# Optimization experiments

Hardware: AMD Instinct MI355X
Metric: run time of the kernel (lower is better)

The kernel has to match this reference:

```python
import jax, jax.numpy as jnp
import numpy as np

B, N, DIM = 4, 1024, 768
HEADS, DIM_HEAD = 12, 64
INNER = HEADS * DIM_HEAD  # 768
SCALE = DIM ** -0.5


def setup_inputs() -> dict:
    key = jax.random.key(0)
    ks = jax.random.split(key, 5)
    return {
        "x": jax.random.normal(ks[0], (B, N, DIM), dtype=jnp.float32),
        "pos_embedding": jax.random.normal(ks[1], (B, N, DIM), dtype=jnp.float32),
        "w_qkv": jax.random.normal(ks[2], (DIM, 3 * INNER), dtype=jnp.float32) * (DIM ** -0.5),
        "w_qk_pos": jax.random.normal(ks[3], (DIM, 2 * INNER), dtype=jnp.float32) * (DIM ** -0.5),
        "w_out": jax.random.normal(ks[4], (INNER, DIM), dtype=jnp.float32) * (INNER ** -0.5),
        "b_out": jnp.zeros((DIM,), dtype=jnp.float32),
    }


def _split_heads(t):
    # [b, n, h*d] -> [b, h, n, d]
    b, n, _ = t.shape
    return t.reshape(b, n, HEADS, DIM_HEAD).transpose(0, 2, 1, 3)


def reference(x, pos_embedding, w_qkv, w_qk_pos, w_out, b_out):
    qkv = x @ w_qkv  # [b, n, 3*inner]
    q, k, v = (_split_heads(t) for t in jnp.split(qkv, 3, axis=-1))
    qk_pos = pos_embedding @ w_qk_pos  # [b, n, 2*inner]
    q_pos, k_pos = (_split_heads(t) for t in jnp.split(qk_pos, 2, axis=-1))

    dots = jnp.einsum('bhid,bhjd->bhij', q, k) * SCALE
    dots_pos = jnp.einsum('bhid,bhjd->bhij', q_pos, k_pos) * SCALE
    dots = (dots + dots_pos) * 0.5  # averaged content+positional scores

    attn = jax.nn.softmax(dots, axis=-1)
    out = jnp.einsum('bhij,bhjd->bhid', attn, v)
    out = out.transpose(0, 2, 1, 3).reshape(x.shape[0], x.shape[1], INNER)
    return out @ w_out + b_out
```

## Files before the change

### kernel.cpp

```cpp
#include <hip/hip_runtime.h>
#include <cstdint>
#include <cstddef>

typedef __bf16 bf16;
typedef __bf16 bf16x8 __attribute__((ext_vector_type(8)));
typedef __bf16 bf16x4v __attribute__((ext_vector_type(4)));
typedef float  f32x4  __attribute__((ext_vector_type(4)));

#define MFMA(a, b, c) __builtin_amdgcn_mfma_f32_16x16x32_bf16((a), (b), (c), 0, 0, 0)

typedef __attribute__((address_space(3))) unsigned int  lds_u32;
typedef __attribute__((address_space(1))) unsigned int glob_u32;


__global__ void k_prep(const float* __restrict__ x, const float* __restrict__ pos,
                       const float* __restrict__ w_qkv, const float* __restrict__ w_qk_pos,
                       const float* __restrict__ w_out,
                       bf16* __restrict__ xb, bf16* __restrict__ posb,
                       bf16* __restrict__ wqkvT, bf16* __restrict__ wqkposT,
                       bf16* __restrict__ woutT) {
    __shared__ float t[32][33];
    const int blk = blockIdx.x;
    if (blk < 6144) {
        int i = blk * 256 + threadIdx.x;
        const float* in = x; bf16* out = xb;
        if (i >= 786432) { i -= 786432; in = pos; out = posb; }
        float4 v = reinterpret_cast<const float4*>(in)[i];
        bf16x4v o; o[0] = (bf16)v.x; o[1] = (bf16)v.y; o[2] = (bf16)v.z; o[3] = (bf16)v.w;
        reinterpret_cast<bf16x4v*>(out)[i] = o;
        return;
    }
    int bx = (blk - 6144) % 144, ky = (blk - 6144) / 144;
    const float* in; bf16* out; int N;
    if (bx < 72)       { in = w_qkv;    out = wqkvT;   N = 2304; }
    else if (bx < 120) { in = w_qk_pos; out = wqkposT; N = 1536; bx -= 72; }
    else               { in = w_out;    out = woutT;   N = 768;  bx -= 120; }
    const int n0 = bx * 32, k0 = ky * 32;
    const int tx = threadIdx.x & 31, ty = threadIdx.x >> 5;
#pragma unroll
    for (int r = 0; r < 32; r += 8)
        t[ty + r][tx] = in[(size_t)(k0 + ty + r) * N + n0 + tx];
    __syncthreads();
#pragma unroll
    for (int r = 0; r < 32; r += 8)
        out[(size_t)(n0 + ty + r) * 768 + k0 + tx] = (bf16)t[tx][ty + r];
}

__launch_bounds__(512, 2)
__global__ void k_gemm12(const bf16* __restrict__ xb, const bf16* __restrict__ posb,
                         const bf16* __restrict__ wqkvT, const bf16* __restrict__ wqkposT,
                         bf16* __restrict__ qcat, bf16* __restrict__ kcat,
                         bf16* __restrict__ vT) {
    __shared__ bf16 lA[2][256][32];
    __shared__ bf16 lB[2][256][32];

    const int tid  = threadIdx.x;
    const int lane = tid & 63, wave = tid >> 6;
    const int quad = lane >> 4, col = lane & 15;
    const int sw2  = (col >> 1) & 3;
    const int wm = (wave >> 2) * 128, wn = (wave & 3) * 64;

    const int fid = blockIdx.x;
    const int xcd = fid & 7, s = fid >> 3;
    const int bx = s % 15;
    const int by = xcd * 2 + s / 15;

    int mode, nBase;
    const bf16 *A, *BT;
    if (bx < 9) { mode = 0; A = xb;   BT = wqkvT;   nBase = bx * 256; }
    else        { mode = 1; A = posb; BT = wqkposT; nBase = (bx - 9) * 256; }
    const int mBase = by * 256;

    const bf16* Ap = A  + (size_t)mBase * 768;
    const bf16* Bp = BT + (size_t)nBase * 768;

#define STAGE12(buf, k0)                                                        \
    _Pragma("unroll")                                                           \
    for (int j = 0; j < 2; ++j) {                                               \
        int idx = (wave * 2 + j) * 64 + lane;                                   \
        int row = idx >> 2, c = (idx & 3) ^ ((row >> 1) & 3);                   \
        __builtin_amdgcn_global_load_lds(                                       \
            (const glob_u32*)(Ap + (size_t)row * 768 + (k0) + c * 8),           \
            (lds_u32*)((char*)&lA[buf][0][0] + (wave * 2 + j) * 1024), 16, 0, 0);\
        __builtin_amdgcn_global_load_lds(                                       \
            (const glob_u32*)(Bp + (size_t)row * 768 + (k0) + c * 8),           \
            (lds_u32*)((char*)&lB[buf][0][0] + (wave * 2 + j) * 1024), 16, 0, 0);\
    }

    f32x4 acc[8][4];
#pragma unroll
    for (int mi = 0; mi < 8; ++mi)
#pragma unroll
        for (int ni = 0; ni < 4; ++ni) acc[mi][ni] = f32x4{0.f, 0.f, 0.f, 0.f};

    STAGE12(0, 0)
    for (int it = 0; it < 24; ++it) {
        const int cur = it & 1, nxt = cur ^ 1;
        __syncthreads();
        if (it < 23) STAGE12(nxt, (it + 1) * 32)

        bf16x8 af[8], bfg[4];
#pragma unroll
        for (int mi = 0; mi < 8; ++mi)
            af[mi]  = *(const bf16x8*)&lA[cur][wm + mi * 16 + col][(quad ^ sw2) * 8];
#pragma unroll
        for (int ni = 0; ni < 4; ++ni)
            bfg[ni] = *(const bf16x8*)&lB[cur][wn + ni * 16 + col][(quad ^ sw2) * 8];
#pragma unroll
        for (int mi = 0; mi < 8; ++mi)
#pragma unroll
            for (int ni = 0; ni < 4; ++ni)
                acc[mi][ni] = MFMA(af[mi], bfg[ni], acc[mi][ni]);
    }
#undef STAGE12

    const float c2s = 0.018042195912f * 1.44269504089f;
    const int bb = mBase >> 10;
    const int sr0 = (mBase & 1023) + wm + quad * 4;
    const int which = (mode == 0) ? (nBase >= 1536 ? 2 : (nBase >= 768 ? 1 : 0))
                                  : (nBase >= 768 ? 1 : 0);
#pragma unroll
    for (int ni = 0; ni < 4; ++ni) {
        const int nb = nBase + wn + ni * 16;
        const int rem = nb - which * 768;
        const int hh = rem >> 6, dd0 = rem & 63;
        const size_t hb = (size_t)(bb * 12 + hh);
        if (mode == 0 && which == 2) {
            bf16* dstv = vT + (hb * 64 + dd0 + col) * 1024 + sr0;
#pragma unroll
            for (int mi = 0; mi < 8; ++mi) {
                bf16x4v pk;
#pragma unroll
                for (int r = 0; r < 4; ++r) pk[r] = (bf16)acc[mi][ni][r];
                *(bf16x4v*)(dstv + mi * 16) = pk;
            }
        } else {
            const float scl = (which == 0) ? c2s : 1.0f;
            bf16* dstq = (which == 0 ? qcat : kcat)
                       + (hb * 1024 + sr0) * 128 + (mode == 1 ? 64 : 0) + dd0 + col;
#pragma unroll
            for (int mi = 0; mi < 8; ++mi)
#pragma unroll
                for (int r = 0; r < 4; ++r)
                    dstq[(size_t)(mi * 16 + r) * 128] = (bf16)(acc[mi][ni][r] * scl);
        }
    }
}

__launch_bounds__(256, 3)
__global__ void k_attn(const bf16* __restrict__ qcat, const bf16* __restrict__ kcat,
                       const bf16* __restrict__ vT, bf16* __restrict__ attn_out) {
    __shared__ bf16 lK[2][64][128];
    __shared__ bf16 lV[2][64][72];

    const int tid  = threadIdx.x;
    const int lane = tid & 63, wave = tid >> 6;
    const int quad = lane >> 4, col = lane & 15;
    const int sw   = col & 7;

    const int fid = blockIdx.x;
    const int xcd = fid & 7, s = fid >> 3;
    const int qt = s & 15;
    const int unit = (s >> 4) * 8 + xcd;
    const int b = unit / 12, h = unit % 12;

    const bf16* Qb = qcat + (size_t)unit * 1024 * 128;
    const bf16* Kb = kcat + (size_t)unit * 1024 * 128;
    const bf16* Vb = vT   + (size_t)unit * 64 * 1024;

    const int kidx = wave * 256 + lane;

#define STAGE_K(buf, kv0)                                                      \
    _Pragma("unroll")                                                          \
    for (int j = 0; j < 4; ++j) {                                              \
        int idx = kidx + j * 64;                                               \
        int row = idx >> 4, c = idx & 15, csrc = c ^ (row & 7);                \
        __builtin_amdgcn_global_load_lds(                                      \
            (const glob_u32*)(Kb + (size_t)((kv0) + row) * 128 + csrc * 8),    \
            (lds_u32*)(&lK[buf][0][0] + (wave * 4 + j) * 512), 16, 0, 0);      \
    }

    int vdj[2], vsk[2], vka[2];
#pragma unroll
    for (int j = 0; j < 2; ++j) {
        int cid = wave * 128 + j * 64 + lane;
        vdj[j] = cid >> 3;
        int sck = cid & 7;
        vsk[j] = sck * 8;
        vka[j] = (sck >> 2) * 32 + (sck & 1) * 16 + ((sck >> 1) & 1) * 4;
    }

#define LOAD_V(kv0)                                                            \
    _Pragma("unroll")                                                          \
    for (int j = 0; j < 2; ++j)                                                \
        vreg[j] = *(const uint4*)(Vb + (size_t)vdj[j] * 1024 + (kv0) + vsk[j]);
#define WRITE_V(buf)                                                           \
    _Pragma("unroll")                                                          \
    for (int j = 0; j < 2; ++j) {                                               \
        *(uint2*)&lV[buf][vdj[j]][vka[j]]     = make_uint2(vreg[j].x, vreg[j].y);\
        *(uint2*)&lV[buf][vdj[j]][vka[j] + 8] = make_uint2(vreg[j].z, vreg[j].w);\
    }

    bf16x8 qb[4];
    {
        const bf16* qrow = Qb + (size_t)(qt * 64 + wave * 16 + col) * 128;
#pragma unroll
        for (int f = 0; f < 4; ++f) qb[f] = *(const bf16x8*)(qrow + f * 32 + quad * 8);
    }

    f32x4 o[4];
#pragma unroll
    for (int vt = 0; vt < 4; ++vt) o[vt] = f32x4{0.f, 0.f, 0.f, 0.f};
    float lsum = 0.f;

    uint4 vreg[2];
    STAGE_K(0, 0)
    LOAD_V(0)
    WRITE_V(0)

    for (int it = 0; it < 16; ++it) {
        const int cur = it & 1, nxt = cur ^ 1;
        __syncthreads();
        if (it < 15) {
            const int kv1 = (it + 1) * 64;
            STAGE_K(nxt, kv1)
            LOAD_V(kv1)
        }

        f32x4 st[4];
#pragma unroll
        for (int t = 0; t < 4; ++t) st[t] = f32x4{0.f, 0.f, 0.f, 0.f};
#pragma unroll
        for (int t = 0; t < 4; ++t)
#pragma unroll
            for (int f = 0; f < 4; ++f) {
                bf16x8 kf = *(const bf16x8*)&lK[cur][t * 16 + col][((f * 4 + quad) ^ sw) * 8];
                st[t] = MFMA(kf, qb[f], st[t]);
            }

        bf16x8 pbf[2];
#pragma unroll
        for (int c = 0; c < 2; ++c) {
#pragma unroll
            for (int r = 0; r < 4; ++r) {
                float p0 = exp2f(st[2 * c][r]);
                float p1 = exp2f(st[2 * c + 1][r]);
                lsum += p0 + p1;
                pbf[c][r]     = (bf16)p0;
                pbf[c][4 + r] = (bf16)p1;
            }
        }

#pragma unroll
        for (int c = 0; c < 2; ++c)
#pragma unroll
            for (int vt = 0; vt < 4; ++vt) {
                bf16x8 vf = *(const bf16x8*)&lV[cur][vt * 16 + col][c * 32 + quad * 8];
                o[vt] = MFMA(vf, pbf[c], o[vt]);
            }

        if (it < 15) WRITE_V(nxt)
    }

    float l = lsum;
    l += __shfl_xor(l, 16, 64);
    l += __shfl_xor(l, 32, 64);
    const float inv = 1.f / l;

    const int qrow = qt * 64 + wave * 16 + col;
    bf16* dst = attn_out + ((size_t)b * 1024 + qrow) * 768 + h * 64;
#pragma unroll
    for (int vt = 0; vt < 4; ++vt) {
        bf16x4v pk;
#pragma unroll
        for (int r = 0; r < 4; ++r) pk[r] = (bf16)(o[vt][r] * inv);
        *(bf16x4v*)(dst + vt * 16 + quad * 4) = pk;
    }
#undef STAGE_K
#undef LOAD_V
#undef WRITE_V
}

__launch_bounds__(256, 3)
__global__ void k_gemm_out(const bf16* __restrict__ aout, const bf16* __restrict__ woutT,
                           const float* __restrict__ bias, float* __restrict__ out) {
    __shared__ bf16 lA[2][64][32];
    __shared__ bf16 lB[2][64][32];

    const int tid  = threadIdx.x;
    const int lane = tid & 63, wave = tid >> 6;
    const int quad = lane >> 4, col = lane & 15;
    const int sw2  = (col >> 1) & 3;
    const int wm = (wave >> 1) * 32, wn = (wave & 1) * 32;

    const int fid = blockIdx.x;
    const int xcd = fid & 7, s = fid >> 3;
    const int bx = s % 12;
    const int by = xcd * 8 + s / 12;

    const int mBase = by * 64, nBase = bx * 64;

    const bf16* Ap = aout  + (size_t)mBase * 768;
    const bf16* Bp = woutT + (size_t)nBase * 768;

#define STAGE_O(buf, k0)                                                        \
    {                                                                           \
        int idx = wave * 64 + lane;                                             \
        int row = idx >> 2, c = (idx & 3) ^ ((row >> 1) & 3);                   \
        __builtin_amdgcn_global_load_lds(                                       \
            (const glob_u32*)(Ap + (size_t)row * 768 + (k0) + c * 8),           \
            (lds_u32*)((char*)&lA[buf][0][0] + wave * 1024), 16, 0, 0);         \
        __builtin_amdgcn_global_load_lds(                                       \
            (const glob_u32*)(Bp + (size_t)row * 768 + (k0) + c * 8),           \
            (lds_u32*)((char*)&lB[buf][0][0] + wave * 1024), 16, 0, 0);         \
    }

    f32x4 acc[2][2];
#pragma unroll
    for (int mi = 0; mi < 2; ++mi)
#pragma unroll
        for (int ni = 0; ni < 2; ++ni) acc[mi][ni] = f32x4{0.f, 0.f, 0.f, 0.f};

    STAGE_O(0, 0)
    for (int it = 0; it < 24; ++it) {
        const int cur = it & 1, nxt = cur ^ 1;
        __syncthreads();
        if (it < 23) STAGE_O(nxt, (it + 1) * 32)

        bf16x8 af[2], bfg[2];
#pragma unroll
        for (int mi = 0; mi < 2; ++mi)
            af[mi]  = *(const bf16x8*)&lA[cur][wm + mi * 16 + col][(quad ^ sw2) * 8];
#pragma unroll
        for (int ni = 0; ni < 2; ++ni)
            bfg[ni] = *(const bf16x8*)&lB[cur][wn + ni * 16 + col][(quad ^ sw2) * 8];
#pragma unroll
        for (int mi = 0; mi < 2; ++mi)
#pragma unroll
            for (int ni = 0; ni < 2; ++ni)
                acc[mi][ni] = MFMA(af[mi], bfg[ni], acc[mi][ni]);
    }
#undef STAGE_O

#pragma unroll
    for (int mi = 0; mi < 2; ++mi)
#pragma unroll
        for (int ni = 0; ni < 2; ++ni)
#pragma unroll
            for (int r = 0; r < 4; ++r) {
                int m = mBase + wm + mi * 16 + quad * 4 + r;
                int n = nBase + wn + ni * 16 + col;
                out[(size_t)m * 768 + n] = acc[mi][ni][r] + bias[n];
            }
}

extern "C" void kernel_launch(void* const* d_in, const int* in_sizes, int n_in,
                              void* d_out, int out_size, void* d_ws, size_t ws_size,
                              hipStream_t stream) {
    const float* x        = (const float*)d_in[0];
    const float* pos      = (const float*)d_in[1];
    const float* w_qkv    = (const float*)d_in[2];
    const float* w_qk_pos = (const float*)d_in[3];
    const float* w_out    = (const float*)d_in[4];
    const float* b_out    = (const float*)d_in[5];
    float* out = (float*)d_out;

    char* ws = (char*)d_ws;
    bf16* xb      = (bf16*)(ws);
    bf16* posb    = (bf16*)(ws + 6291456);
    bf16* wqkvT   = (bf16*)(ws + 12582912);
    bf16* wqkposT = (bf16*)(ws + 16121856);
    bf16* woutT   = (bf16*)(ws + 18481152);
    bf16* qcat    = (bf16*)(ws + 19660800);
    bf16* kcat    = (bf16*)(ws + 32243712);
    bf16* vT      = (bf16*)(ws + 44826624);
    bf16* aout    = (bf16*)(ws + 51118080);

    k_prep<<<9600, 256, 0, stream>>>(x, pos, w_qkv, w_qk_pos, w_out,
                                     xb, posb, wqkvT, wqkposT, woutT);
    k_gemm12<<<240, 512, 0, stream>>>(xb, posb, wqkvT, wqkposT, qcat, kcat, vT);
    k_attn<<<768, 256, 0, stream>>>(qcat, kcat, vT, aout);
    k_gemm_out<<<768, 256, 0, stream>>>(aout, woutT, b_out, out);
}
```

Before: 182.3 us.

## Restructure QKV projection GEMM into 8-wave ping-pong pipeline with quadrant-split LDS

Rewrites the main loop of the QKV/positional projection GEMM. The K step grows from 32 to 64 and the LDS tiles are split into halves, so each wave loads its A/B quadrant fragments and issues MFMA sub-blocks between explicit barriers, while global-to-LDS loads for later K tiles are spread across the phases. This is meant to overlap global loads, LDS reads and MFMA more finely than the old double-buffer loop. Separately, s_setprio is raised around MFMA clusters in both the GEMM and the attention kernel to favour matrix issue. The barrier and waitcnt choreography is complex and a mistake could cause data races, and the many barriers add sync overhead.

```diff
diff --git a/kernel.cpp b/kernel.cpp
--- a/kernel.cpp
+++ b/kernel.cpp
@@ -51,14 +51,18 @@
                          const bf16* __restrict__ wqkvT, const bf16* __restrict__ wqkposT,
                          bf16* __restrict__ qcat, bf16* __restrict__ kcat,
                          bf16* __restrict__ vT) {
-    __shared__ bf16 lA[2][256][32];
-    __shared__ bf16 lB[2][256][32];
+    __shared__ bf16 lA[2][2][2][128][32];
+    __shared__ bf16 lB[2][2][2][128][32];
 
     const int tid  = threadIdx.x;
     const int lane = tid & 63, wave = tid >> 6;
     const int quad = lane >> 4, col = lane & 15;
     const int sw2  = (col >> 1) & 3;
-    const int wm = (wave >> 2) * 128, wn = (wave & 3) * 64;
+    const int rg8  = (quad ^ sw2) * 8;
+    const int mh   = wave >> 2;
+    const int nh   = (wave >> 1) & 1;
+    const int nb64 = (wave & 1) * 64;
+    const int wm   = mh * 128, wn = (wave & 3) * 64;
 
     const int fid = blockIdx.x;
     const int xcd = fid & 7, s = fid >> 3;
@@ -74,18 +78,53 @@
     const bf16* Ap = A  + (size_t)mBase * 768;
     const bf16* Bp = BT + (size_t)nBase * 768;
 
-#define STAGE12(buf, k0)                                                        \
-    _Pragma("unroll")                                                           \
-    for (int j = 0; j < 2; ++j) {                                               \
-        int idx = (wave * 2 + j) * 64 + lane;                                   \
-        int row = idx >> 2, c = (idx & 3) ^ ((row >> 1) & 3);                   \
-        __builtin_amdgcn_global_load_lds(                                       \
-            (const glob_u32*)(Ap + (size_t)row * 768 + (k0) + c * 8),           \
-            (lds_u32*)((char*)&lA[buf][0][0] + (wave * 2 + j) * 1024), 16, 0, 0);\
-        __builtin_amdgcn_global_load_lds(                                       \
-            (const glob_u32*)(Bp + (size_t)row * 768 + (k0) + c * 8),           \
-            (lds_u32*)((char*)&lB[buf][0][0] + (wave * 2 + j) * 1024), 16, 0, 0);\
-    }
+#define STAGE_A8(ss, h, t)                                                     \
+    _Pragma("unroll")                                                          \
+    for (int j = 0; j < 2; ++j) {                                              \
+        int c = (lane & 3) ^ ((lane >> 3) & 3);                                \
+        __builtin_amdgcn_global_load_lds(                                      \
+            (const glob_u32*)(Ap + (size_t)((h) * 128 + wave * 16 + (lane >> 2)) * 768 \
+                              + (t) * 64 + j * 32 + c * 8),                    \
+            (lds_u32*)(&lA[ss][h][j][wave * 16][0]), 16, 0, 0);                \
+    }
+#define STAGE_B8(ss, h, t)                                                     \
+    _Pragma("unroll")                                                          \
+    for (int j = 0; j < 2; ++j) {                                              \
+        int c = (lane & 3) ^ ((lane >> 3) & 3);                                \
+        __builtin_amdgcn_global_load_lds(                                      \
+            (const glob_u32*)(Bp + (size_t)((h) * 128 + wave * 16 + (lane >> 2)) * 768 \
+                              + (t) * 64 + j * 32 + c * 8),                    \
+            (lds_u32*)(&lB[ss][h][j][wave * 16][0]), 16, 0, 0);                \
+    }
+
+#define READ_A8(ss, mq)                                                        \
+    _Pragma("unroll")                                                          \
+    for (int f = 0; f < 4; ++f)                                                \
+    _Pragma("unroll")                                                          \
+    for (int ks = 0; ks < 2; ++ks)                                             \
+        afr[f][ks] = *(const bf16x8*)&lA[ss][mh][ks][(mq) * 64 + f * 16 + col][rg8];
+#define READ_B8(ss, nq)                                                        \
+    _Pragma("unroll")                                                          \
+    for (int n = 0; n < 2; ++n)                                                \
+    _Pragma("unroll")                                                          \
+    for (int ks = 0; ks < 2; ++ks)                                             \
+        bfr[n][ks] = *(const bf16x8*)&lB[ss][nh][ks][nb64 + (nq) * 32 + n * 16 + col][rg8];
+
+#define MM16(mq, nq)                                                           \
+    __builtin_amdgcn_s_setprio(1);                                             \
+    _Pragma("unroll")                                                          \
+    for (int ks = 0; ks < 2; ++ks)                                             \
+    _Pragma("unroll")                                                          \
+    for (int f = 0; f < 4; ++f)                                                \
+    _Pragma("unroll")                                                          \
+    for (int n = 0; n < 2; ++n)                                                \
+        acc[(mq) * 4 + f][(nq) * 2 + n] =                                      \
+            MFMA(afr[f][ks], bfr[n][ks], acc[(mq) * 4 + f][(nq) * 2 + n]);     \
+    __builtin_amdgcn_s_setprio(0);
+
+#define BAR()   __builtin_amdgcn_s_barrier()
+#define LGKM0() do { asm volatile("s_waitcnt lgkmcnt(0)" ::: "memory");        \
+                     __builtin_amdgcn_sched_barrier(0); } while (0)
 
     f32x4 acc[8][4];
 #pragma unroll
@@ -93,26 +132,65 @@
 #pragma unroll
         for (int ni = 0; ni < 4; ++ni) acc[mi][ni] = f32x4{0.f, 0.f, 0.f, 0.f};
 
-    STAGE12(0, 0)
-    for (int it = 0; it < 24; ++it) {
-        const int cur = it & 1, nxt = cur ^ 1;
-        __syncthreads();
-        if (it < 23) STAGE12(nxt, (it + 1) * 32)
-
-        bf16x8 af[8], bfg[4];
-#pragma unroll
-        for (int mi = 0; mi < 8; ++mi)
-            af[mi]  = *(const bf16x8*)&lA[cur][wm + mi * 16 + col][(quad ^ sw2) * 8];
-#pragma unroll
-        for (int ni = 0; ni < 4; ++ni)
-            bfg[ni] = *(const bf16x8*)&lB[cur][wn + ni * 16 + col][(quad ^ sw2) * 8];
-#pragma unroll
-        for (int mi = 0; mi < 8; ++mi)
-#pragma unroll
-            for (int ni = 0; ni < 4; ++ni)
-                acc[mi][ni] = MFMA(af[mi], bfg[ni], acc[mi][ni]);
-    }
-#undef STAGE12
+    bf16x8 afr[4][2], bfr[2][2];
+
+    STAGE_A8(0, 0, 0) STAGE_A8(0, 1, 0)
+    STAGE_B8(0, 0, 0)
+    STAGE_B8(0, 1, 0)
+    STAGE_A8(1, 0, 1) STAGE_A8(1, 1, 1)
+    asm volatile("s_waitcnt vmcnt(4)" ::: "memory");
+    BAR();
+
+    for (int i = 0; i < 6; ++i) {
+        const int tO = 2 * i + 1, tE2 = 2 * i + 2, tO2 = 2 * i + 3;
+        READ_A8(0, 0) READ_B8(0, 0)
+        STAGE_B8(1, 0, tO)
+        BAR(); LGKM0();
+        MM16(0, 0)
+        BAR();
+        READ_B8(0, 1)
+        STAGE_B8(1, 1, tO)
+        BAR(); LGKM0();
+        MM16(0, 1)
+        BAR();
+        READ_A8(0, 1)
+        BAR(); LGKM0();
+        MM16(1, 1)
+        BAR();
+        READ_B8(0, 0)
+        BAR(); LGKM0();
+        MM16(1, 0)
+        asm volatile("s_waitcnt vmcnt(0)" ::: "memory");
+        BAR();
+        READ_A8(1, 0) READ_B8(1, 0)
+        if (i < 5) { STAGE_A8(0, 0, tE2) STAGE_A8(0, 1, tE2) }
+        BAR(); LGKM0();
+        MM16(0, 0)
+        BAR();
+        READ_B8(1, 1)
+        if (i < 5) STAGE_B8(0, 1, tE2)
+        BAR(); LGKM0();
+        MM16(0, 1)
+        BAR();
+        READ_A8(1, 1)
+        if (i < 5) STAGE_B8(0, 0, tE2)
+        BAR(); LGKM0();
+        MM16(1, 1)
+        BAR();
+        READ_B8(1, 0)
+        if (i < 5) { STAGE_A8(1, 0, tO2) STAGE_A8(1, 1, tO2) }
+        BAR(); LGKM0();
+        MM16(1, 0)
+        if (i < 5) { asm volatile("s_waitcnt vmcnt(4)" ::: "memory"); }
+        BAR();
+    }
+#undef STAGE_A8
+#undef STAGE_B8
+#undef READ_A8
+#undef READ_B8
+#undef MM16
+#undef BAR
+#undef LGKM0
 
     const float c2s = 0.018042195912f * 1.44269504089f;
     const int bb = mBase >> 10;
@@ -230,6 +308,7 @@
         f32x4 st[4];
 #pragma unroll
         for (int t = 0; t < 4; ++t) st[t] = f32x4{0.f, 0.f, 0.f, 0.f};
+        __builtin_amdgcn_s_setprio(1);
 #pragma unroll
         for (int t = 0; t < 4; ++t)
 #pragma unroll
@@ -237,6 +316,7 @@
                 bf16x8 kf = *(const bf16x8*)&lK[cur][t * 16 + col][((f * 4 + quad) ^ sw) * 8];
                 st[t] = MFMA(kf, qb[f], st[t]);
             }
+        __builtin_amdgcn_s_setprio(0);
 
         bf16x8 pbf[2];
 #pragma unroll
@@ -251,6 +331,7 @@
             }
         }
 
+        __builtin_amdgcn_s_setprio(1);
 #pragma unroll
         for (int c = 0; c < 2; ++c)
 #pragma unroll
@@ -258,6 +339,7 @@
                 bf16x8 vf = *(const bf16x8*)&lV[cur][vt * 16 + col][c * 32 + quad * 8];
                 o[vt] = MFMA(vf, pbf[c], o[vt]);
             }
+        __builtin_amdgcn_s_setprio(0);
 
         if (it < 15) WRITE_V(nxt)
     }
```

Measured after the change: 173.2 us. 5.0% less time.
